# Performance work log

Measured on AMD Instinct MI355X. Metric: run time of the kernel, lower is better.

The kernel has to match this reference:

```python
import jax, jax.numpy as jnp
import numpy as np

B = 32; H = 56; W = 56; DIM = 384; HEADS = 12; WIN = 7; SHIFT = 3
HEAD_DIM = DIM // HEADS; SCALE = HEAD_DIM ** -0.5
N = WIN * WIN; NW = (H // WIN) * (W // WIN); L = H * W + 1; HID = 4 * DIM


def _rel_index():
    coords = np.stack(np.meshgrid(np.arange(WIN), np.arange(WIN), indexing='ij')).reshape(2, -1)
    rel = (coords[:, :, None] - coords[:, None, :]).transpose(1, 2, 0)
    rel[:, :, 0] += WIN - 1
    rel[:, :, 1] += WIN - 1
    rel[:, :, 0] *= 2 * WIN - 1
    return jnp.asarray(rel.sum(-1))  # (N, N) int


def _attn_mask():
    # standard Swin shift mask, padded with a zero column so the cls key is always visible
    img = np.zeros((H, W))
    sl = (slice(0, -WIN), slice(-WIN, -SHIFT), slice(-SHIFT, None))
    cnt = 0
    for hs in sl:
        for ws in sl:
            img[hs, ws] = cnt
            cnt += 1
    mw = img.reshape(H // WIN, WIN, W // WIN, WIN).transpose(0, 2, 1, 3).reshape(-1, N)
    m = mw[:, None, :] - mw[:, :, None]
    m = np.where(m != 0, -100.0, 0.0).astype(np.float32)
    m = np.pad(m, ((0, 0), (0, 0), (1, 0)))  # (nW, N, N+1)
    return jnp.asarray(m)


REL_INDEX = _rel_index()
ATTN_MASK = _attn_mask()


def _ln(x, g, b, eps=1e-5):
    m = x.mean(-1, keepdims=True)
    v = ((x - m) ** 2).mean(-1, keepdims=True)
    return (x - m) * jax.lax.rsqrt(v + eps) * g + b


def setup_inputs() -> dict:
    key = jax.random.key(0)
    ks = jax.random.split(key, 6)
    s = 0.02
    return dict(
        x=jax.random.normal(ks[0], (B, L, DIM), jnp.float32),
        norm1_g=jnp.ones((DIM,), jnp.float32), norm1_b=jnp.zeros((DIM,), jnp.float32),
        qkv_w=jax.random.normal(ks[1], (3 * DIM, DIM), jnp.float32) * s,
        qkv_b=jnp.zeros((3 * DIM,), jnp.float32),
        rel_bias_table=jax.random.normal(ks[2], ((2 * WIN - 1) ** 2, HEADS), jnp.float32) * s,
        proj_w=jax.random.normal(ks[3], (DIM, DIM), jnp.float32) * s,
        proj_b=jnp.zeros((DIM,), jnp.float32),
        norm2_g=jnp.ones((DIM,), jnp.float32), norm2_b=jnp.zeros((DIM,), jnp.float32),
        fc1_w=jax.random.normal(ks[4], (HID, DIM), jnp.float32) * s,
        fc1_b=jnp.zeros((HID,), jnp.float32),
        fc2_w=jax.random.normal(ks[5], (DIM, HID), jnp.float32) * s,
        fc2_b=jnp.zeros((DIM,), jnp.float32),
    )


def reference(x, norm1_g, norm1_b, qkv_w, qkv_b, rel_bias_table, proj_w, proj_b,
              norm2_g, norm2_b, fc1_w, fc1_b, fc2_w, fc2_b):
    Bx = x.shape[0]
    shortcut = x
    h = _ln(x, norm1_g, norm1_b)
    qkv = h @ qkv_w.T + qkv_b  # (B, L, 3C)

    # ---- global cls attention: token 0 attends to every token (ClsAttention) ----
    t = qkv.reshape(Bx, L, 3, HEADS, HEAD_DIM).transpose(2, 0, 3, 1, 4)  # (3, B, h, L, d)
    q0 = t[0, :, :, 0:1, :] * SCALE
    cls_attn = jax.nn.softmax(jnp.einsum('bhqd,bhkd->bhqk', q0, t[1]), axis=-1)
    cls_out = jnp.einsum('bhqk,bhkd->bhqd', cls_attn, t[2]).transpose(0, 2, 1, 3).reshape(Bx, 1, DIM)

    # ---- shifted-window attention for patch tokens, cls qkv prepended per window ----
    cls_qkv = qkv[:, :1]  # (B, 1, 3C)
    p = qkv[:, 1:].reshape(Bx, H, W, 3 * DIM)
    p = jnp.roll(p, (-SHIFT, -SHIFT), axis=(1, 2))
    pw = p.reshape(Bx, H // WIN, WIN, W // WIN, WIN, 3 * DIM).transpose(0, 1, 3, 2, 4, 5)
    pw = pw.reshape(Bx * NW, N, 3 * DIM)
    cls_rep = jnp.broadcast_to(cls_qkv[:, None], (Bx, NW, 1, 3 * DIM)).reshape(Bx * NW, 1, 3 * DIM)
    qkvw = jnp.concatenate([cls_rep, pw], axis=1)  # (B*nW, N+1, 3C)

    tw = qkvw.reshape(Bx * NW, N + 1, 3, HEADS, HEAD_DIM).transpose(2, 0, 3, 1, 4)
    q = tw[0, :, :, 1:, :] * SCALE  # patch queries (B*nW, h, N, d)
    attn = jnp.einsum('bhqd,bhkd->bhqk', q, tw[1])  # (B*nW, h, N, N+1)
    rel = rel_bias_table[REL_INDEX.reshape(-1)].reshape(N, N, HEADS).transpose(2, 0, 1)
    attn = jnp.concatenate([attn[..., :1], attn[..., 1:] + rel[None]], axis=-1)
    attn = attn.reshape(Bx, NW, HEADS, N, N + 1) + ATTN_MASK[None, :, None]
    attn = jax.nn.softmax(attn.reshape(Bx * NW, HEADS, N, N + 1), axis=-1)
    xw = jnp.einsum('bhqk,bhkd->bhqd', attn, tw[2]).transpose(0, 2, 1, 3).reshape(Bx * NW, N, DIM)

    # window reverse + reverse cyclic shift
    xp = xw.reshape(Bx, H // WIN, W // WIN, WIN, WIN, DIM).transpose(0, 1, 3, 2, 4, 5).reshape(Bx, H, W, DIM)
    xp = jnp.roll(xp, (SHIFT, SHIFT), axis=(1, 2)).reshape(Bx, H * W, DIM)

    a = jnp.concatenate([cls_out, xp], axis=1) @ proj_w.T + proj_b
    x1 = shortcut + a
    h2 = _ln(x1, norm2_g, norm2_b)
    h2 = jax.nn.gelu(h2 @ fc1_w.T + fc1_b, approximate=False)
    return x1 + (h2 @ fc2_w.T + fc2_b)
```

## Files before the change

### kernel.cpp

```cpp
#include <hip/hip_runtime.h>

#define DEVI __device__ __forceinline__

typedef __attribute__((ext_vector_type(8))) __bf16 bf16x8;
typedef __attribute__((ext_vector_type(4))) float f32x4;
typedef unsigned short u16;
typedef unsigned int u32;

static constexpr int kB = 32;
static constexpr int kL = 3137;
static constexpr int kM = kB * kL;
static constexpr int kHeads = 12;
static constexpr float kScale = 0.17677669529663687f;
static constexpr int kNC = 13;

DEVI u16 f2b(float f) {
  u32 u = __float_as_uint(f);
  u32 r = (u + 0x7fffu + ((u >> 16) & 1u)) >> 16;
  return (u16)r;
}
DEVI float blo(u32 u) { return __uint_as_float(u << 16); }
DEVI float bhi(u32 u) { return __uint_as_float(u & 0xffff0000u); }
DEVI float b2f(u16 h) { return __uint_as_float(((u32)h) << 16); }

DEVI void async16(const void* g, void* l) {
  __builtin_amdgcn_global_load_lds((const __attribute__((address_space(1))) u32*)g,
                                   (__attribute__((address_space(3))) u32*)l, 16, 0, 0);
}

DEVI float wred_max(float v) {
#pragma unroll
  for (int o = 32; o; o >>= 1) v = fmaxf(v, __shfl_xor(v, o));
  return v;
}
DEVI float wred_sum(float v) {
#pragma unroll
  for (int o = 32; o; o >>= 1) v += __shfl_xor(v, o);
  return v;
}

__global__ void cvt_all(const float* __restrict__ a, const float* __restrict__ b,
                        const float* __restrict__ c2, const float* __restrict__ d,
                        u16* __restrict__ oa, u16* __restrict__ ob,
                        u16* __restrict__ oc, u16* __restrict__ od) {
  int i = blockIdx.x * 256 + threadIdx.x;
  if (i < 442368) oa[i] = f2b(a[i]);
  else if (i < 589824) ob[i - 442368] = f2b(b[i - 442368]);
  else if (i < 1179648) oc[i - 589824] = f2b(c2[i - 589824]);
  else od[i - 1179648] = f2b(d[i - 1179648]);
}

__global__ __launch_bounds__(256)
void ln384(const float* __restrict__ x, const float* __restrict__ gam,
           const float* __restrict__ bet, u16* __restrict__ out, int rows) {
  int row = blockIdx.x * 4 + (threadIdx.x >> 6);
  if (row >= rows) return;
  int lane = threadIdx.x & 63;
  const float2* xr = (const float2*)(x + (size_t)row * 384);
  float2 v[3];
  float s = 0.f, s2 = 0.f;
#pragma unroll
  for (int i = 0; i < 3; i++) {
    v[i] = xr[lane + 64 * i];
    s += v[i].x + v[i].y;
    s2 += v[i].x * v[i].x + v[i].y * v[i].y;
  }
  s = wred_sum(s);
  s2 = wred_sum(s2);
  float mean = s * (1.f / 384.f);
  float var = s2 * (1.f / 384.f) - mean * mean;
  float rinv = rsqrtf(var + 1e-5f);
  const float2* gp = (const float2*)gam;
  const float2* bp = (const float2*)bet;
  u32* orow = (u32*)(out + (size_t)row * 384);
#pragma unroll
  for (int i = 0; i < 3; i++) {
    int idx = lane + 64 * i;
    float2 gg = gp[idx], bb = bp[idx];
    float lo = (v[i].x - mean) * rinv * gg.x + bb.x;
    float hi = (v[i].y - mean) * rinv * gg.y + bb.y;
    orow[idx] = (u32)f2b(lo) | ((u32)f2b(hi) << 16);
  }
}

__global__ __launch_bounds__(256)
void ln384b(const u16* __restrict__ x, const float* __restrict__ gam,
            const float* __restrict__ bet, u16* __restrict__ out, int rows) {
  int row = blockIdx.x * 4 + (threadIdx.x >> 6);
  if (row >= rows) return;
  int lane = threadIdx.x & 63;
  const u32* xr = (const u32*)(x + (size_t)row * 384);
  float vl[3], vh[3];
  float s = 0.f, s2 = 0.f;
#pragma unroll
  for (int i = 0; i < 3; i++) {
    u32 u = xr[lane + 64 * i];
    vl[i] = blo(u); vh[i] = bhi(u);
    s += vl[i] + vh[i];
    s2 += vl[i] * vl[i] + vh[i] * vh[i];
  }
  s = wred_sum(s);
  s2 = wred_sum(s2);
  float mean = s * (1.f / 384.f);
  float var = s2 * (1.f / 384.f) - mean * mean;
  float rinv = rsqrtf(var + 1e-5f);
  const float2* gp = (const float2*)gam;
  const float2* bp = (const float2*)bet;
  u32* orow = (u32*)(out + (size_t)row * 384);
#pragma unroll
  for (int i = 0; i < 3; i++) {
    int idx = lane + 64 * i;
    float2 gg = gp[idx], bb = bp[idx];
    float lo = (vl[i] - mean) * rinv * gg.x + bb.x;
    float hi = (vh[i] - mean) * rinv * gg.y + bb.y;
    orow[idx] = (u32)f2b(lo) | ((u32)f2b(hi) << 16);
  }
}

DEVI float gelu_exact(float v) { return 0.5f * v * (1.f + erff(v * 0.70710678118654752f)); }

template <int EPI>
__global__ __launch_bounds__(256)
void gemm_bt(const u16* __restrict__ A, const u16* __restrict__ W,
             const float* __restrict__ bias, const void* __restrict__ resv,
             void* __restrict__ outp, int M, int N, int K, int NX, int TMv) {
  const int nwg = gridDim.x;
  const int orig = blockIdx.x;
  const int xcd = orig & 7, rest = orig >> 3;
  const int q8 = nwg >> 3, r8 = nwg & 7;
  const int id = ((xcd < r8) ? xcd * (q8 + 1) : r8 * (q8 + 1) + (xcd - r8) * q8) + rest;
  const int col0 = (id % NX) * 128;
  const int rowG = (id / NX) * TMv * 128;

  const int tid = threadIdx.x, lane = tid & 63, wv = tid >> 6;
  __shared__ __align__(16) u16 As[3][128 * 32];
  __shared__ __align__(16) u16 Bs[3][128 * 32];
  const int wm = wv >> 1, wn = wv & 1;
  const int c = lane & 15, g = lane >> 4;
  const int NT = K >> 5;

  const int rr = lane >> 2;
  const int gnat = (lane & 3) ^ ((lane >> 3) & 3);

  auto stage = [&](int t2, int k2, int bfi) {
    int kk = k2 * 32 + gnat * 8;
    int rbase = rowG + t2 * 128;
#pragma unroll
    for (int s = 0; s < 2; s++) {
      int ch = wv * 2 + s;
      int r = ch * 16 + rr;
      async16(A + (size_t)min(rbase + r, M - 1) * K + kk, &As[bfi][ch * 512]);
      async16(W + (size_t)min(col0 + r, N - 1) * K + kk, &Bs[bfi][ch * 512]);
    }
  };

  int cc[4];
  float bv[4];
#pragma unroll
  for (int n = 0; n < 4; n++) {
    cc[n] = col0 + wn * 64 + n * 16 + c;
    bv[n] = bias[cc[n]];
  }

  stage(0, 0, 0);
  stage(0, 1, 1);
  int cur = 0;
  for (int t = 0; t < TMv; ++t) {
    f32x4 acc[4][4];
    f32x4 zero = {0.f, 0.f, 0.f, 0.f};
#pragma unroll
    for (int m = 0; m < 4; m++)
#pragma unroll
      for (int n = 0; n < 4; n++) acc[m][n] = zero;

    for (int kt = 0; kt < NT; ++kt) {
      if (t == TMv - 1 && kt == NT - 1) asm volatile("s_waitcnt vmcnt(0)" ::: "memory");
      else                              asm volatile("s_waitcnt vmcnt(4)" ::: "memory");
      __builtin_amdgcn_s_barrier();
      {
        int kt2 = kt + 2, t2 = t;
        if (kt2 >= NT) { kt2 -= NT; t2++; }
        if (t2 < TMv) {
          int nb = cur + 2; if (nb >= 3) nb -= 3;
          stage(t2, kt2, nb);
        }
      }
      bf16x8 af[4], bw[4];
#pragma unroll
      for (int m = 0; m < 4; m++) {
        int row = wm * 64 + m * 16 + c;
        af[m] = *(const bf16x8*)&As[cur][row * 32 + ((g ^ ((row >> 1) & 3)) << 3)];
      }
#pragma unroll
      for (int n = 0; n < 4; n++) {
        int row = wn * 64 + n * 16 + c;
        bw[n] = *(const bf16x8*)&Bs[cur][row * 32 + ((g ^ ((row >> 1) & 3)) << 3)];
      }
      __builtin_amdgcn_s_setprio(1);
#pragma unroll
      for (int m = 0; m < 4; m++)
#pragma unroll
        for (int n = 0; n < 4; n++)
          acc[m][n] = __builtin_amdgcn_mfma_f32_16x16x32_bf16(af[m], bw[n], acc[m][n], 0, 0, 0);
      __builtin_amdgcn_s_setprio(0);
      cur = cur + 1; if (cur >= 3) cur -= 3;
    }

    int rowT = rowG + t * 128;
#pragma unroll
    for (int m = 0; m < 4; m++) {
      int rb = rowT + wm * 64 + m * 16 + (g << 2);
#pragma unroll
      for (int j = 0; j < 4; j++) {
        int r = rb + j;
        if (r < M) {
#pragma unroll
          for (int n = 0; n < 4; n++) {
            float vv = acc[m][n][j] + bv[n];
            size_t off = (size_t)r * N + cc[n];
            if constexpr (EPI == 0) {
              ((u16*)outp)[off] = f2b(vv);
            } else if constexpr (EPI == 2) {
              ((u16*)outp)[off] = f2b(gelu_exact(vv));
            } else if constexpr (EPI == 3) {
              ((u16*)outp)[off] = f2b(vv + ((const float*)resv)[off]);
            } else {
              ((float*)outp)[off] = vv + b2f(((const u16*)resv)[off]);
            }
          }
        }
      }
    }
  }
}

__global__ __launch_bounds__(256)
void cls_part(const u16* __restrict__ qkv, float* __restrict__ parts) {
  int bh = blockIdx.x;
  int chunk = blockIdx.y;
  int b = bh / kHeads, h = bh % kHeads;
  __shared__ float qs[32];
  __shared__ float ps[256];
  __shared__ float red[8];
  __shared__ float part[8][32];
  int tid = threadIdx.x, lane = tid & 63, wv = tid >> 6;
  size_t rb = (size_t)b * kL;
  if (tid < 32) qs[tid] = b2f(qkv[rb * 1152 + h * 32 + tid]) * kScale;
  __syncthreads();
  int t0 = chunk * 256;
  int nTok = min(256, kL - t0);
  float s = -1e30f;
  if (tid < nTok) {
    const u16* kp = qkv + (rb + t0 + tid) * 1152 + 384 + h * 32;
    s = 0.f;
#pragma unroll
    for (int g4 = 0; g4 < 4; g4++) {
      uint4 u = *(const uint4*)(kp + g4 * 8);
      s += qs[g4*8+0]*blo(u.x) + qs[g4*8+1]*bhi(u.x)
         + qs[g4*8+2]*blo(u.y) + qs[g4*8+3]*bhi(u.y)
         + qs[g4*8+4]*blo(u.z) + qs[g4*8+5]*bhi(u.z)
         + qs[g4*8+6]*blo(u.w) + qs[g4*8+7]*bhi(u.w);
    }
  }
  float m = wred_max(s);
  if (lane == 0) red[wv] = m;
  __syncthreads();
  float gm = fmaxf(fmaxf(red[0], red[1]), fmaxf(red[2], red[3]));
  float p = (tid < nTok) ? __expf(s - gm) : 0.f;
  ps[tid] = p;
  float ls = wred_sum(p);
  if (lane == 0) red[4 + wv] = ls;
  __syncthreads();
  float tot = red[4] + red[5] + red[6] + red[7];
  int d = tid & 31, g = tid >> 5;
  float a = 0.f;
  for (int t = g; t < nTok; t += 8)
    a += ps[t] * b2f(qkv[(rb + t0 + t) * 1152 + 768 + h * 32 + d]);
  part[g][d] = a;
  __syncthreads();
  if (tid < 32) {
    float o = 0.f;
#pragma unroll
    for (int g2 = 0; g2 < 8; g2++) o += part[g2][tid];
    float* pp = parts + ((size_t)bh * kNC + chunk) * 34;
    pp[2 + tid] = o;
    if (tid == 0) { pp[0] = gm; pp[1] = tot; }
  }
}

__global__ __launch_bounds__(64)
void cls_reduce(const float* __restrict__ parts, u16* __restrict__ aout) {
  int bh = blockIdx.x;
  int b = bh / kHeads, h = bh % kHeads;
  int tid = threadIdx.x;
  __shared__ float sm[kNC], ss[kNC];
  if (tid < kNC) {
    sm[tid] = parts[((size_t)bh * kNC + tid) * 34];
    ss[tid] = parts[((size_t)bh * kNC + tid) * 34 + 1];
  }
  __syncthreads();
  float M = -1e30f;
#pragma unroll
  for (int c = 0; c < kNC; c++) M = fmaxf(M, sm[c]);
  float W = 0.f;
#pragma unroll
  for (int c = 0; c < kNC; c++) W += ss[c] * __expf(sm[c] - M);
  if (tid < 32) {
    float o = 0.f;
#pragma unroll
    for (int c = 0; c < kNC; c++)
      o += parts[((size_t)bh * kNC + c) * 34 + 2 + tid] * __expf(sm[c] - M);
    aout[(size_t)b * kL * 384 + h * 32 + tid] = f2b(o / W);
  }
}

__global__ __launch_bounds__(256)
void bias_pre(const float* __restrict__ relb, float* __restrict__ bf) {
  int blk = blockIdx.x;
  int cls = blk / 12, h = blk % 12;
  int clsH = (cls >> 1) & 1, clsW = cls & 1;
  for (int idx = threadIdx.x; idx < 4096; idx += 256) {
    int k = idx >> 6, q = idx & 63;
    float v = 0.f;
    if (k >= 50) {
      v = -1e9f;
    } else if (k >= 1 && q < 49) {
      int kt = k - 1, ki = kt / 7, kj = kt % 7;
      int qi = q / 7, qj = q % 7;
      v = relb[((qi - ki + 6) * 13 + (qj - kj + 6)) * 12 + h];
      int rq = (clsH ? (qi < 4 ? 1 : 2) : 0) * 3 + (clsW ? (qj < 4 ? 1 : 2) : 0);
      int rk = (clsH ? (ki < 4 ? 1 : 2) : 0) * 3 + (clsW ? (kj < 4 ? 1 : 2) : 0);
      if (rq != rk) v -= 100.f;
    }
    bf[(size_t)blk * 4096 + idx] = v;
  }
}

__global__ __launch_bounds__(256)
void win_attn2(const u16* __restrict__ qkv, const float* __restrict__ biasf,
               u16* __restrict__ aout) {
  const int tid = threadIdx.x, lane = tid & 63, wv = tid >> 6;
  const int gid = blockIdx.x * 4 + wv;
  const int h = gid % 12;
  const int wr = gid / 12;
  const int win = wr & 63, b = wr >> 6;
  const int wi = win >> 3, wj = win & 7;
  const int cls = ((wi == 7) ? 2 : 0) + ((wj == 7) ? 1 : 0);
  const int c = lane & 15, g = lane >> 4;

  __shared__ __align__(16) u16 KS[4][64 * 40];
  __shared__ __align__(16) u16 VT[4][32 * 72];
  __shared__ int RW[4][52];
  u16* Ks = KS[wv];
  u16* Vt = VT[wv];
  int* Rows = RW[wv];

#pragma unroll
  for (int it = 0; it < 2; ++it) {
    int idx = it * 64 + lane;
    int tok = idx >> 1, half = idx & 1;
    if (tok < 50) {
      int row;
      if (tok == 0) {
        row = b * kL;
      } else {
        int n = tok - 1;
        int i = n / 7, j = n % 7;
        int r = wi * 7 + i, c2 = wj * 7 + j;
        int orr = r + 3; if (orr >= 56) orr -= 56;
        int occ = c2 + 3; if (occ >= 56) occ -= 56;
        row = b * kL + 1 + orr * 56 + occ;
      }
      if (half == 0) Rows[tok] = row;
      const u16* base = qkv + (size_t)row * 1152 + h * 32 + half * 16;
      uint4 k0 = *(const uint4*)(base + 384);
      uint4 k1 = *(const uint4*)(base + 384 + 8);
      *(uint4*)&Ks[tok * 40 + half * 16] = k0;
      *(uint4*)&Ks[tok * 40 + half * 16 + 8] = k1;
      uint4 v0 = *(const uint4*)(base + 768);
      uint4 v1 = *(const uint4*)(base + 768 + 8);
      u32 vw[8] = {v0.x, v0.y, v0.z, v0.w, v1.x, v1.y, v1.z, v1.w};
#pragma unroll
      for (int m = 0; m < 8; ++m) {
        Vt[(half * 16 + m * 2 + 0) * 72 + tok] = (u16)(vw[m] & 0xffffu);
        Vt[(half * 16 + m * 2 + 1) * 72 + tok] = (u16)(vw[m] >> 16);
      }
    } else {
      uint4 z = {0u, 0u, 0u, 0u};
      *(uint4*)&Ks[tok * 40 + half * 16] = z;
      *(uint4*)&Ks[tok * 40 + half * 16 + 8] = z;
#pragma unroll
      for (int m = 0; m < 16; ++m) Vt[(half * 16 + m) * 72 + tok] = 0;
    }
  }
  __syncthreads();

  bf16x8 qf[4];
#pragma unroll
  for (int nt = 0; nt < 4; ++nt) {
    int q = nt * 16 + c;
    if (q > 48) q = 48;
    const u16* qp = qkv + (size_t)Rows[q + 1] * 1152 + h * 32 + g * 8;
    qf[nt] = *(const bf16x8*)qp;
  }

  f32x4 s[4][4];
  {
    f32x4 z = {0.f, 0.f, 0.f, 0.f};
    bf16x8 kf[4];
#pragma unroll
    for (int mt = 0; mt < 4; ++mt)
      kf[mt] = *(const bf16x8*)&Ks[(mt * 16 + c) * 40 + g * 8];
#pragma unroll
    for (int mt = 0; mt < 4; ++mt)
#pragma unroll
      for (int nt = 0; nt < 4; ++nt)
        s[mt][nt] = __builtin_amdgcn_mfma_f32_16x16x32_bf16(kf[mt], qf[nt], z, 0, 0, 0);
  }

  const float* bp = biasf + (size_t)(cls * 12 + h) * 4096;
  u32 wq[4][8];
#pragma unroll
  for (int nt = 0; nt < 4; ++nt) {
    float pv[16];
#pragma unroll
    for (int mt = 0; mt < 4; ++mt)
#pragma unroll
      for (int r = 0; r < 4; ++r)
        pv[mt * 4 + r] = s[mt][nt][r] * kScale + bp[(mt * 16 + g * 4 + r) * 64 + nt * 16 + c];
    float mx = pv[0];
#pragma unroll
    for (int i2 = 1; i2 < 16; ++i2) mx = fmaxf(mx, pv[i2]);
    mx = fmaxf(mx, __shfl_xor(mx, 16));
    mx = fmaxf(mx, __shfl_xor(mx, 32));
    float sum = 0.f;
#pragma unroll
    for (int i2 = 0; i2 < 16; ++i2) { pv[i2] = __expf(pv[i2] - mx); sum += pv[i2]; }
    sum += __shfl_xor(sum, 16);
    sum += __shfl_xor(sum, 32);
    float rs = 1.f / sum;
#pragma unroll
    for (int i2 = 0; i2 < 16; ++i2) pv[i2] *= rs;
#pragma unroll
    for (int mt = 0; mt < 4; ++mt) {
      u32 w0, w1;
      asm("v_cvt_pk_bf16_f32 %0, %1, %2" : "=v"(w0) : "v"(pv[mt * 4 + 0]), "v"(pv[mt * 4 + 1]));
      asm("v_cvt_pk_bf16_f32 %0, %1, %2" : "=v"(w1) : "v"(pv[mt * 4 + 2]), "v"(pv[mt * 4 + 3]));
      wq[nt][mt * 2 + 0] = w0;
      wq[nt][mt * 2 + 1] = w1;
    }
  }

  bf16x8 pa[4][2];
#pragma unroll
  for (int mt2 = 0; mt2 < 4; ++mt2)
#pragma unroll
    for (int ks = 0; ks < 2; ++ks) {
      union { u32 u[4]; bf16x8 v; } cvt;
#pragma unroll
      for (int wj2 = 0; wj2 < 4; ++wj2) {
        int srcLane = c + 16 * (((g & 1) << 1) + (wj2 >> 1));
        u32 a0 = (u32)__shfl((int)wq[mt2][(2 * ks + 0) * 2 + (wj2 & 1)], srcLane);
        u32 a1 = (u32)__shfl((int)wq[mt2][(2 * ks + 1) * 2 + (wj2 & 1)], srcLane);
        cvt.u[wj2] = (g < 2) ? a0 : a1;
      }
      pa[mt2][ks] = cvt.v;
    }

  f32x4 o[4][2];
  f32x4 z2 = {0.f, 0.f, 0.f, 0.f};
#pragma unroll
  for (int mt2 = 0; mt2 < 4; ++mt2)
#pragma unroll
    for (int ntd = 0; ntd < 2; ++ntd) o[mt2][ntd] = z2;
#pragma unroll
  for (int ks = 0; ks < 2; ++ks) {
    bf16x8 vf[2];
#pragma unroll
    for (int ntd = 0; ntd < 2; ++ntd)
      vf[ntd] = *(const bf16x8*)&Vt[(ntd * 16 + c) * 72 + ks * 32 + g * 8];
#pragma unroll
    for (int mt2 = 0; mt2 < 4; ++mt2)
#pragma unroll
      for (int ntd = 0; ntd < 2; ++ntd)
        o[mt2][ntd] = __builtin_amdgcn_mfma_f32_16x16x32_bf16(pa[mt2][ks], vf[ntd], o[mt2][ntd], 0, 0, 0);
  }

#pragma unroll
  for (int mt2 = 0; mt2 < 4; ++mt2)
#pragma unroll
    for (int r = 0; r < 4; ++r) {
      int q = mt2 * 16 + g * 4 + r;
      if (q < 49) {
        int row = Rows[q + 1];
        u16* op = aout + (size_t)row * 384 + h * 32 + c;
        op[0]  = f2b(o[mt2][0][r]);
        op[16] = f2b(o[mt2][1][r]);
      }
    }
}

extern "C" void kernel_launch(void* const* d_in, const int* in_sizes, int n_in,
                              void* d_out, int out_size, void* d_ws, size_t ws_size,
                              hipStream_t stream) {
  const float* x      = (const float*)d_in[0];
  const float* n1g    = (const float*)d_in[1];
  const float* n1b    = (const float*)d_in[2];
  const float* qkv_w  = (const float*)d_in[3];
  const float* qkv_b  = (const float*)d_in[4];
  const float* relb   = (const float*)d_in[5];
  const float* proj_w = (const float*)d_in[6];
  const float* proj_b = (const float*)d_in[7];
  const float* n2g    = (const float*)d_in[8];
  const float* n2b    = (const float*)d_in[9];
  const float* fc1_w  = (const float*)d_in[10];
  const float* fc1_b  = (const float*)d_in[11];
  const float* fc2_w  = (const float*)d_in[12];
  const float* fc2_b  = (const float*)d_in[13];
  float* out = (float*)d_out;
  char* ws = (char*)d_ws;

  u16* wqkv  = (u16*)(ws + 0);
  float* biasf = (float*)(ws + 0);
  u16* wproj = (u16*)(ws + 884736);
  u16* wfc1  = (u16*)(ws + 1179648);
  u16* wfc2  = (u16*)(ws + 2359296);
  u16* qkvb  = (u16*)(ws + 3538944);
  u16* x1b   = (u16*)(ws + 3538944);
  u16* h2b   = (u16*)(ws + 80633856);
  u16* gb    = (u16*)(ws + 119181312);
  u16* hbuf  = (u16*)(ws + 234823680);
  float* parts = (float*)d_out;

  cvt_all<<<6912, 256, 0, stream>>>(qkv_w, proj_w, fc1_w, fc2_w, wqkv, wproj, wfc1, wfc2);

  ln384<<<(kM + 3) / 4, 256, 0, stream>>>(x, n1g, n1b, hbuf, kM);
  gemm_bt<0><<<9 * 197, 256, 0, stream>>>(hbuf, wqkv, qkv_b, nullptr, qkvb, kM, 1152, 384, 9, 4);
  bias_pre<<<48, 256, 0, stream>>>(relb, biasf);
  cls_part<<<dim3(kB * kHeads, kNC), 256, 0, stream>>>(qkvb, parts);
  cls_reduce<<<kB * kHeads, 64, 0, stream>>>(parts, hbuf);
  win_attn2<<<kB * 64 * kHeads / 4, 256, 0, stream>>>(qkvb, biasf, hbuf);
  gemm_bt<3><<<3 * 393, 256, 0, stream>>>(hbuf, wproj, proj_b, x, x1b, kM, 384, 384, 3, 2);

  for (int c = 0; c < 2; c++) {
    int r0 = c * 50192, nr = 50192;
    ln384b<<<(nr + 3) / 4, 256, 0, stream>>>(x1b + (size_t)r0 * 384, n2g, n2b, h2b, nr);
    gemm_bt<2><<<12 * 99, 256, 0, stream>>>(h2b, wfc1, fc1_b, nullptr, gb, nr, 1536, 384, 12, 4);
    gemm_bt<4><<<3 * 393, 256, 0, stream>>>(gb, wfc2, fc2_b, x1b + (size_t)r0 * 384,
                                            out + (size_t)r0 * 384, nr, 384, 1536, 3, 1);
  }
}
```

Before: 971.6 us.

## Fuse cls-token attention partials into window attention kernel

Removes the separate cls_part kernel, which re-read K and V for all 3137 tokens from global memory. Instead, each window-attention wavefront computes the cls query's partial softmax over its window's keys (already staged in LDS) and writes max, sum and weighted V partials, with the cls key counted only in window 0. A 64-chunk reduce kernel then combines the partials per batch and head. The cost is extra work inside win_attn2 (a serial 50-step loop and one more LDS array), and the reduce now runs after win_attn2 rather than before it.

```diff
diff --git a/kernel.cpp b/kernel.cpp
--- a/kernel.cpp
+++ b/kernel.cpp
@@ -12,7 +12,6 @@
 static constexpr int kM = kB * kL;
 static constexpr int kHeads = 12;
 static constexpr float kScale = 0.17677669529663687f;
-static constexpr int kNC = 13;
 
 DEVI u16 f2b(float f) {
   u32 u = __float_as_uint(f);
@@ -234,83 +233,23 @@
   }
 }
 
-__global__ __launch_bounds__(256)
-void cls_part(const u16* __restrict__ qkv, float* __restrict__ parts) {
-  int bh = blockIdx.x;
-  int chunk = blockIdx.y;
-  int b = bh / kHeads, h = bh % kHeads;
-  __shared__ float qs[32];
-  __shared__ float ps[256];
-  __shared__ float red[8];
-  __shared__ float part[8][32];
-  int tid = threadIdx.x, lane = tid & 63, wv = tid >> 6;
-  size_t rb = (size_t)b * kL;
-  if (tid < 32) qs[tid] = b2f(qkv[rb * 1152 + h * 32 + tid]) * kScale;
-  __syncthreads();
-  int t0 = chunk * 256;
-  int nTok = min(256, kL - t0);
-  float s = -1e30f;
-  if (tid < nTok) {
-    const u16* kp = qkv + (rb + t0 + tid) * 1152 + 384 + h * 32;
-    s = 0.f;
-#pragma unroll
-    for (int g4 = 0; g4 < 4; g4++) {
-      uint4 u = *(const uint4*)(kp + g4 * 8);
-      s += qs[g4*8+0]*blo(u.x) + qs[g4*8+1]*bhi(u.x)
-         + qs[g4*8+2]*blo(u.y) + qs[g4*8+3]*bhi(u.y)
-         + qs[g4*8+4]*blo(u.z) + qs[g4*8+5]*bhi(u.z)
-         + qs[g4*8+6]*blo(u.w) + qs[g4*8+7]*bhi(u.w);
-    }
-  }
-  float m = wred_max(s);
-  if (lane == 0) red[wv] = m;
-  __syncthreads();
-  float gm = fmaxf(fmaxf(red[0], red[1]), fmaxf(red[2], red[3]));
-  float p = (tid < nTok) ? __expf(s - gm) : 0.f;
-  ps[tid] = p;
-  float ls = wred_sum(p);
-  if (lane == 0) red[4 + wv] = ls;
-  __syncthreads();
-  float tot = red[4] + red[5] + red[6] + red[7];
-  int d = tid & 31, g = tid >> 5;
-  float a = 0.f;
-  for (int t = g; t < nTok; t += 8)
-    a += ps[t] * b2f(qkv[(rb + t0 + t) * 1152 + 768 + h * 32 + d]);
-  part[g][d] = a;
-  __syncthreads();
-  if (tid < 32) {
-    float o = 0.f;
-#pragma unroll
-    for (int g2 = 0; g2 < 8; g2++) o += part[g2][tid];
-    float* pp = parts + ((size_t)bh * kNC + chunk) * 34;
-    pp[2 + tid] = o;
-    if (tid == 0) { pp[0] = gm; pp[1] = tot; }
-  }
-}
-
 __global__ __launch_bounds__(64)
-void cls_reduce(const float* __restrict__ parts, u16* __restrict__ aout) {
+void cls_reduce64(const float* __restrict__ parts, u16* __restrict__ aout) {
   int bh = blockIdx.x;
   int b = bh / kHeads, h = bh % kHeads;
-  int tid = threadIdx.x;
-  __shared__ float sm[kNC], ss[kNC];
-  if (tid < kNC) {
-    sm[tid] = parts[((size_t)bh * kNC + tid) * 34];
-    ss[tid] = parts[((size_t)bh * kNC + tid) * 34 + 1];
-  }
-  __syncthreads();
-  float M = -1e30f;
-#pragma unroll
-  for (int c = 0; c < kNC; c++) M = fmaxf(M, sm[c]);
-  float W = 0.f;
-#pragma unroll
-  for (int c = 0; c < kNC; c++) W += ss[c] * __expf(sm[c] - M);
-  if (tid < 32) {
+  int lane = threadIdx.x;
+  __shared__ float sm[64];
+  const float* base = parts + (size_t)bh * 64 * 34;
+  float m = base[lane * 34];
+  float e = base[lane * 34 + 1];
+  sm[lane] = m;
+  float M = wred_max(m);
+  float W = wred_sum(e * __expf(m - M));
+  if (lane < 32) {
     float o = 0.f;
-#pragma unroll
-    for (int c = 0; c < kNC; c++)
-      o += parts[((size_t)bh * kNC + c) * 34 + 2 + tid] * __expf(sm[c] - M);
-    aout[(size_t)b * kL * 384 + h * 32 + tid] = f2b(o / W);
+    for (int c2 = 0; c2 < 64; c2++)
+      o += base[c2 * 34 + 2 + lane] * __expf(sm[c2] - M);
+    aout[(size_t)b * kL * 384 + h * 32 + lane] = f2b(o / W);
   }
 }
 
@@ -338,7 +277,7 @@
 
 __global__ __launch_bounds__(256)
 void win_attn2(const u16* __restrict__ qkv, const float* __restrict__ biasf,
-               u16* __restrict__ aout) {
+               u16* __restrict__ aout, float* __restrict__ parts) {
   const int tid = threadIdx.x, lane = tid & 63, wv = tid >> 6;
   const int gid = blockIdx.x * 4 + wv;
   const int h = gid % 12;
@@ -351,9 +290,11 @@
   __shared__ __align__(16) u16 KS[4][64 * 40];
   __shared__ __align__(16) u16 VT[4][32 * 72];
   __shared__ int RW[4][52];
+  __shared__ float FP[4][52];
   u16* Ks = KS[wv];
   u16* Vt = VT[wv];
   int* Rows = RW[wv];
+  float* Fp = FP[wv];
 
 #pragma unroll
   for (int it = 0; it < 2; ++it) {
@@ -394,6 +335,36 @@
     }
   }
   __syncthreads();
+
+  {
+    if (lane < 32)
+      Fp[lane] = b2f(qkv[(size_t)(b * kL) * 1152 + h * 32 + lane]) * kScale;
+    float sc = -1e30f;
+    if (lane <= 49 && (lane >= 1 || win == 0)) {
+      sc = 0.f;
+      const u16* kr = &Ks[lane * 40];
+#pragma unroll
+      for (int d4 = 0; d4 < 4; d4++) {
+        uint4 u = *(const uint4*)(kr + d4 * 8);
+        sc += Fp[d4*8+0]*blo(u.x) + Fp[d4*8+1]*bhi(u.x)
+            + Fp[d4*8+2]*blo(u.y) + Fp[d4*8+3]*bhi(u.y)
+            + Fp[d4*8+4]*blo(u.z) + Fp[d4*8+5]*bhi(u.z)
+            + Fp[d4*8+6]*blo(u.w) + Fp[d4*8+7]*bhi(u.w);
+      }
+    }
+    float mloc = wred_max(sc);
+    float pcls = (sc > -1e29f) ? __expf(sc - mloc) : 0.f;
+    float esum = wred_sum(pcls);
+    if (lane < 50) Fp[lane] = pcls;
+    float* pp = parts + (size_t)((b * 12 + h) * 64 + win) * 34;
+    if (lane == 0) { pp[0] = mloc; pp[1] = esum; }
+    if (lane < 32) {
+      float o = 0.f;
+      for (int t = 0; t < 50; t++)
+        o += Fp[t] * b2f(Vt[lane * 72 + t]);
+      pp[2 + lane] = o;
+    }
+  }
 
   bf16x8 qf[4];
 #pragma unroll
@@ -537,9 +508,8 @@
   ln384<<<(kM + 3) / 4, 256, 0, stream>>>(x, n1g, n1b, hbuf, kM);
   gemm_bt<0><<<9 * 197, 256, 0, stream>>>(hbuf, wqkv, qkv_b, nullptr, qkvb, kM, 1152, 384, 9, 4);
   bias_pre<<<48, 256, 0, stream>>>(relb, biasf);
-  cls_part<<<dim3(kB * kHeads, kNC), 256, 0, stream>>>(qkvb, parts);
-  cls_reduce<<<kB * kHeads, 64, 0, stream>>>(parts, hbuf);
-  win_attn2<<<kB * 64 * kHeads / 4, 256, 0, stream>>>(qkvb, biasf, hbuf);
+  win_attn2<<<kB * 64 * kHeads / 4, 256, 0, stream>>>(qkvb, biasf, hbuf, parts);
+  cls_reduce64<<<kB * kHeads, 64, 0, stream>>>(parts, hbuf);
   gemm_bt<3><<<3 * 393, 256, 0, stream>>>(hbuf, wproj, proj_b, x, x1b, kM, 384, 384, 3, 2);
 
   for (int c = 0; c < 2; c++) {
```

Result: faster. 923.0 us (-5.0%).
